# Optimization experiments

Measured on AMD Instinct MI355X. Metric: run time of the kernel, lower is better.

## Reference

```python
import jax, jax.numpy as jnp
import numpy as np

BITS = 12
MB = BITS - 1                      # mantissa bits
MAX_VAL = 1.0 - 2.0 ** (-MB)       # superfloat max representable magnitude
DENOM = float(2 ** MB - 1)


def sf_decode(enc):
    # enc: int32. NOTE: faithful to source, including its sign convention
    # decoded * (2*sign - 1) where sign=1 for negative inputs (flips sign).
    mantissa = enc & ((1 << MB) - 1)
    sign = (enc >> MB) & 1
    mag = mantissa.astype(jnp.float32) / DENOM * MAX_VAL
    return mag * (2 * sign - 1).astype(jnp.float32)


def sf_encode(x):
    c = jnp.clip(x, -MAX_VAL, MAX_VAL)
    oor = jnp.abs(x) > MAX_VAL
    mantissa = jnp.floor(jnp.abs(c) * DENOM / MAX_VAL).astype(jnp.int32)
    sign = (c < 0).astype(jnp.int32)
    return (mantissa | (sign << MB)), oor


def setup_inputs() -> dict:
    key = jax.random.key(0)
    k1, k2, k3, k4, k5 = jax.random.split(key, 5)
    T, IN, OUT = 512, 4096, 11008
    x = jax.random.normal(k1, (T, IN), dtype=jnp.float32)
    weight_full = jax.random.normal(k2, (OUT, IN), dtype=jnp.float32) * 0.02
    scale = jnp.ones((OUT,), dtype=jnp.float32)
    bias = jax.random.normal(k3, (OUT,), dtype=jnp.float32) * 0.01
    encoded_weight = jax.random.randint(k4, (OUT, IN), 0, 2 ** BITS, dtype=jnp.int32)
    outlier_mask = jax.random.uniform(k5, (OUT, IN)) < 0.005
    return {"x": x, "weight_full": weight_full, "scale": scale, "bias": bias,
            "encoded_weight": encoded_weight, "outlier_mask": outlier_mask}


def reference(x, weight_full, scale, bias, encoded_weight, outlier_mask):
    # decode packed superfloat weight, scatter outliers, rescale per-row
    w = sf_decode(encoded_weight)                       # [OUT, IN]
    w = jnp.where(outlier_mask, weight_full, w)         # == w[mask] = weight[mask]
    w = w * scale[:, None]
    # quantize activations (encode then decode)
    enc_x, _ = sf_encode(x)
    xq = sf_decode(enc_x)                               # [T, IN]
    return xq @ w.T + bias                              # [T, OUT]
```

## Files before the change

### kernel.cpp

```cpp
#include <hip/hip_runtime.h>
#include <hip/hip_bf16.h>
#include <stdint.h>

#define T_DIM 512
#define IN_DIM 4096
#define OUT_DIM 11008

typedef __attribute__((ext_vector_type(8))) __bf16 bf16x8;
typedef __attribute__((ext_vector_type(8))) short shortx8;
typedef __attribute__((ext_vector_type(4))) float f32x4;

__device__ __forceinline__ short f32_to_bf16_bits(float f) {
    uint32_t x = __builtin_bit_cast(uint32_t, f);
    x += 0x7FFFu + ((x >> 16) & 1u);
    return (short)(x >> 16);
}

__global__ __launch_bounds__(256) void encode_x_kernel(const float* __restrict__ x,
                                                       short* __restrict__ xq) {
    const float MAXV = 2047.0f / 2048.0f;
    int i = (blockIdx.x * 256 + threadIdx.x) * 8;
    float4 a = *(const float4*)(x + i);
    float4 b = *(const float4*)(x + i + 4);
    float v[8] = {a.x, a.y, a.z, a.w, b.x, b.y, b.z, b.w};
    union { short s[8]; int4 v4; } u;
#pragma unroll
    for (int j = 0; j < 8; ++j) {
        float xv = v[j];
        float ax = fminf(fabsf(xv), MAXV);
        float m = floorf(ax * 2047.0f / MAXV);
        float q = m * (1.0f / 2048.0f) * (xv < 0.0f ? 1.0f : -1.0f);
        u.s[j] = f32_to_bf16_bits(q);
    }
    *(int4*)(xq + i) = u.v4;
}

__global__ __launch_bounds__(256) void decode_w_kernel(const int* __restrict__ enc,
                                                       const int* __restrict__ mask,
                                                       const float* __restrict__ wf,
                                                       const float* __restrict__ scale,
                                                       short* __restrict__ wq) {
    int i = (blockIdx.x * 256 + threadIdx.x) * 8;
    int row = i >> 12;
    float s = scale[row];
    int4 e0 = *(const int4*)(enc + i);
    int4 e1 = *(const int4*)(enc + i + 4);
    int4 m0 = *(const int4*)(mask + i);
    int4 m1 = *(const int4*)(mask + i + 4);
    int e[8]  = {e0.x, e0.y, e0.z, e0.w, e1.x, e1.y, e1.z, e1.w};
    int mk[8] = {m0.x, m0.y, m0.z, m0.w, m1.x, m1.y, m1.z, m1.w};
    union { short s[8]; int4 v4; } u;
#pragma unroll
    for (int j = 0; j < 8; ++j) {
        int ev = e[j];
        float v = (float)(ev & 2047) * (1.0f / 2048.0f) * (((ev >> 11) & 1) ? 1.0f : -1.0f);
        if (mk[j]) v = wf[i + j];
        u.s[j] = f32_to_bf16_bits(v * s);
    }
    *(int4*)(wq + i) = u.v4;
}

#define BM 128
#define BN 128
#define BK 32
#define KITERS (IN_DIM / BK)

__global__ __launch_bounds__(256) void gemm_bt_kernel(const short* __restrict__ A,
                                                      const short* __restrict__ B,
                                                      const float* __restrict__ bias,
                                                      float* __restrict__ C) {
    __shared__ short As[BM * BK];
    __shared__ short Bs[BN * BK];
    const int tid  = threadIdx.x;
    const int wave = tid >> 6;
    const int lane = tid & 63;
    const int bn = blockIdx.x, bm = blockIdx.y;

    const int f0 = tid * 8;
    const int r0 = f0 >> 5, c0 = f0 & 31;
    const int f1 = (256 + tid) * 8;
    const int r1 = f1 >> 5, c1 = f1 & 31;
    const short* gA0 = A + (size_t)(bm * BM + r0) * IN_DIM + c0;
    const short* gA1 = A + (size_t)(bm * BM + r1) * IN_DIM + c1;
    const short* gB0 = B + (size_t)(bn * BN + r0) * IN_DIM + c0;
    const short* gB1 = B + (size_t)(bn * BN + r1) * IN_DIM + c1;
    short* lA0 = As + (wave * 64) * 8;
    short* lA1 = As + (256 + wave * 64) * 8;
    short* lB0 = Bs + (wave * 64) * 8;
    short* lB1 = Bs + (256 + wave * 64) * 8;

    const int wm = (wave >> 1) * 64;
    const int wn = (wave & 1) * 64;
    const int quad = lane >> 4;
    const int lr   = lane & 15;

    f32x4 acc[4][4] = {};

    for (int kt = 0; kt < KITERS; ++kt) {
        const int ko = kt * BK;
        __builtin_amdgcn_global_load_lds((__attribute__((address_space(1))) void*)(gA0 + ko),
                                         (__attribute__((address_space(3))) void*)lA0, 16, 0, 0);
        __builtin_amdgcn_global_load_lds((__attribute__((address_space(1))) void*)(gA1 + ko),
                                         (__attribute__((address_space(3))) void*)lA1, 16, 0, 0);
        __builtin_amdgcn_global_load_lds((__attribute__((address_space(1))) void*)(gB0 + ko),
                                         (__attribute__((address_space(3))) void*)lB0, 16, 0, 0);
        __builtin_amdgcn_global_load_lds((__attribute__((address_space(1))) void*)(gB1 + ko),
                                         (__attribute__((address_space(3))) void*)lB1, 16, 0, 0);
        __syncthreads();

        bf16x8 af[4], bfr[4];
#pragma unroll
        for (int mi = 0; mi < 4; ++mi)
            af[mi] = __builtin_bit_cast(bf16x8,
                *(const shortx8*)(As + (wm + mi * 16 + lr) * BK + quad * 8));
#pragma unroll
        for (int ni = 0; ni < 4; ++ni)
            bfr[ni] = __builtin_bit_cast(bf16x8,
                *(const shortx8*)(Bs + (wn + ni * 16 + lr) * BK + quad * 8));
#pragma unroll
        for (int mi = 0; mi < 4; ++mi)
#pragma unroll
            for (int ni = 0; ni < 4; ++ni)
                acc[mi][ni] = __builtin_amdgcn_mfma_f32_16x16x32_bf16(
                    af[mi], bfr[ni], acc[mi][ni], 0, 0, 0);
        __syncthreads();
    }

    const int rowb = bm * BM + wm + quad * 4;
    const int colb = bn * BN + wn + lr;
#pragma unroll
    for (int ni = 0; ni < 4; ++ni) {
        const int col = colb + ni * 16;
        const float bv = bias[col];
#pragma unroll
        for (int mi = 0; mi < 4; ++mi) {
#pragma unroll
            for (int r = 0; r < 4; ++r) {
                const int row = rowb + mi * 16 + r;
                C[(size_t)row * OUT_DIM + col] = acc[mi][ni][r] + bv;
            }
        }
    }
}

extern "C" void kernel_launch(void* const* d_in, const int* in_sizes, int n_in,
                              void* d_out, int out_size, void* d_ws, size_t ws_size,
                              hipStream_t stream) {
    const float* x     = (const float*)d_in[0];
    const float* wf    = (const float*)d_in[1];
    const float* scale = (const float*)d_in[2];
    const float* bias  = (const float*)d_in[3];
    const int*   enc   = (const int*)d_in[4];
    const int*   mask  = (const int*)d_in[5];
    float* out = (float*)d_out;

    short* xq = (short*)d_ws;
    short* wq = (short*)d_ws + (size_t)T_DIM * IN_DIM;

    encode_x_kernel<<<(T_DIM * IN_DIM) / (256 * 8), 256, 0, stream>>>(x, xq);
    decode_w_kernel<<<((size_t)OUT_DIM * IN_DIM) / (256 * 8), 256, 0, stream>>>(
        enc, mask, wf, scale, wq);
    dim3 grid(OUT_DIM / BN, T_DIM / BM);
    gemm_bt_kernel<<<grid, 256, 0, stream>>>(xq, wq, bias, out);
}
```

Measured before the change: 555.0 us.

## Fuse weight dequantization into GEMM with full-T column blocks

The separate weight-decode kernel and its bf16 workspace round trip are removed. Each block now owns 32 output columns across all 512 tokens: it dequantizes enc/mask/outlier weights into a double-buffered, XOR-swizzled LDS tile while MFMAs consume the previous tile, and it reads activation fragments straight from global memory. The intent is to stream the large int32 weight and mask arrays exactly once, with non-temporal loads, and to overlap that streaming with compute. The cost is that activations are re-read from global/L2 by every one of the 344 blocks, and there are few blocks with high register pressure.

Result: slower. 667.6 us (+20.3%).

```diff
diff --git a/kernel.cpp b/kernel.cpp
--- a/kernel.cpp
+++ b/kernel.cpp
@@ -6,9 +6,15 @@
 #define IN_DIM 4096
 #define OUT_DIM 11008
 
+#define BN 32
+#define BK 64
+#define KSTEPS (IN_DIM / BK)
+#define NBLK (OUT_DIM / BN)
+
 typedef __attribute__((ext_vector_type(8))) __bf16 bf16x8;
 typedef __attribute__((ext_vector_type(8))) short shortx8;
 typedef __attribute__((ext_vector_type(4))) float f32x4;
+typedef __attribute__((ext_vector_type(4))) int   intx4;
 
 __device__ __forceinline__ short f32_to_bf16_bits(float f) {
     uint32_t x = __builtin_bit_cast(uint32_t, f);
@@ -35,105 +41,135 @@
     *(int4*)(xq + i) = u.v4;
 }
 
-__global__ __launch_bounds__(256) void decode_w_kernel(const int* __restrict__ enc,
-                                                       const int* __restrict__ mask,
-                                                       const float* __restrict__ wf,
-                                                       const float* __restrict__ scale,
-                                                       short* __restrict__ wq) {
-    int i = (blockIdx.x * 256 + threadIdx.x) * 8;
-    int row = i >> 12;
-    float s = scale[row];
-    int4 e0 = *(const int4*)(enc + i);
-    int4 e1 = *(const int4*)(enc + i + 4);
-    int4 m0 = *(const int4*)(mask + i);
-    int4 m1 = *(const int4*)(mask + i + 4);
-    int e[8]  = {e0.x, e0.y, e0.z, e0.w, e1.x, e1.y, e1.z, e1.w};
-    int mk[8] = {m0.x, m0.y, m0.z, m0.w, m1.x, m1.y, m1.z, m1.w};
-    union { short s[8]; int4 v4; } u;
-#pragma unroll
-    for (int j = 0; j < 8; ++j) {
-        int ev = e[j];
-        float v = (float)(ev & 2047) * (1.0f / 2048.0f) * (((ev >> 11) & 1) ? 1.0f : -1.0f);
-        if (mk[j]) v = wf[i + j];
-        u.s[j] = f32_to_bf16_bits(v * s);
-    }
-    *(int4*)(wq + i) = u.v4;
-}
+__global__ __launch_bounds__(256, 2) void fused_dq_gemm_kernel(
+    const short* __restrict__ A,
+    const int*   __restrict__ enc,
+    const int*   __restrict__ mask,
+    const float* __restrict__ wf,
+    const float* __restrict__ scale,
+    const float* __restrict__ bias,
+    float*       __restrict__ C)
+{
+    __shared__ short Ws[2][BN * BK];
 
-#define BM 128
-#define BN 128
-#define BK 32
-#define KITERS (IN_DIM / BK)
-
-__global__ __launch_bounds__(256) void gemm_bt_kernel(const short* __restrict__ A,
-                                                      const short* __restrict__ B,
-                                                      const float* __restrict__ bias,
-                                                      float* __restrict__ C) {
-    __shared__ short As[BM * BK];
-    __shared__ short Bs[BN * BK];
     const int tid  = threadIdx.x;
     const int wave = tid >> 6;
     const int lane = tid & 63;
-    const int bn = blockIdx.x, bm = blockIdx.y;
-
-    const int f0 = tid * 8;
-    const int r0 = f0 >> 5, c0 = f0 & 31;
-    const int f1 = (256 + tid) * 8;
-    const int r1 = f1 >> 5, c1 = f1 & 31;
-    const short* gA0 = A + (size_t)(bm * BM + r0) * IN_DIM + c0;
-    const short* gA1 = A + (size_t)(bm * BM + r1) * IN_DIM + c1;
-    const short* gB0 = B + (size_t)(bn * BN + r0) * IN_DIM + c0;
-    const short* gB1 = B + (size_t)(bn * BN + r1) * IN_DIM + c1;
-    short* lA0 = As + (wave * 64) * 8;
-    short* lA1 = As + (256 + wave * 64) * 8;
-    short* lB0 = Bs + (wave * 64) * 8;
-    short* lB1 = Bs + (256 + wave * 64) * 8;
-
-    const int wm = (wave >> 1) * 64;
-    const int wn = (wave & 1) * 64;
     const int quad = lane >> 4;
     const int lr   = lane & 15;
+    const int wm   = wave * 128;
+    const int bn   = blockIdx.x;
 
-    f32x4 acc[4][4] = {};
+    const int wrow = tid >> 3;
+    const int q8   = tid & 7;
+    const int grow = bn * BN + wrow;
+    const float s     = scale[grow];
+    const float s2048 = s * (1.0f / 2048.0f);
+    const int*   ep = enc  + (size_t)grow * IN_DIM + q8 * 8;
+    const int*   mp = mask + (size_t)grow * IN_DIM + q8 * 8;
+    const float* wp = wf   + (size_t)grow * IN_DIM + q8 * 8;
+    char* wsw_base = (char*)&Ws[0][0] +
+        (((wrow * (BK * 2) + q8 * 16) ^ ((wrow & 7) << 4)));
 
-    for (int kt = 0; kt < KITERS; ++kt) {
-        const int ko = kt * BK;
-        __builtin_amdgcn_global_load_lds((__attribute__((address_space(1))) void*)(gA0 + ko),
-                                         (__attribute__((address_space(3))) void*)lA0, 16, 0, 0);
-        __builtin_amdgcn_global_load_lds((__attribute__((address_space(1))) void*)(gA1 + ko),
-                                         (__attribute__((address_space(3))) void*)lA1, 16, 0, 0);
-        __builtin_amdgcn_global_load_lds((__attribute__((address_space(1))) void*)(gB0 + ko),
-                                         (__attribute__((address_space(3))) void*)lB0, 16, 0, 0);
-        __builtin_amdgcn_global_load_lds((__attribute__((address_space(1))) void*)(gB1 + ko),
-                                         (__attribute__((address_space(3))) void*)lB1, 16, 0, 0);
-        __syncthreads();
+    const short* pa = A + (size_t)(wm + lr) * IN_DIM + quad * 8;
 
-        bf16x8 af[4], bfr[4];
+    f32x4 acc[8][2] = {};
+
+    auto WS_FRAG = [&](int rb, int ni, int kf) -> bf16x8 {
+        const int row  = ni * 16 + lr;
+        const int byte = ((row * (BK * 2) + quad * 16 + kf * 64) ^ ((row & 7) << 4))
+                         + rb * (BN * BK * 2);
+        return __builtin_bit_cast(bf16x8, *(const shortx8*)((const char*)&Ws[0][0] + byte));
+    };
+
+    auto DQW = [&](const intx4 E0, const intx4 E1, const int* mv, const float* wv, int wb) {
+        int ev[8] = {E0[0], E0[1], E0[2], E0[3], E1[0], E1[1], E1[2], E1[3]};
+        union { short h[8]; int4 q4; } u;
 #pragma unroll
-        for (int mi = 0; mi < 4; ++mi)
-            af[mi] = __builtin_bit_cast(bf16x8,
-                *(const shortx8*)(As + (wm + mi * 16 + lr) * BK + quad * 8));
+        for (int j = 0; j < 8; ++j) {
+            float d = (float)(ev[j] & 2047);
+            if (!(ev[j] & 2048)) d = -d;
+            float v = d * s2048;
+            if (mv[j]) v = wv[j] * s;
+            u.h[j] = f32_to_bf16_bits(v);
+        }
+        *(int4*)(wsw_base + wb * (BN * BK * 2)) = u.q4;
+    };
+
+    intx4 eA0, eA1, mA0, mA1, eB0, eB1, mB0, mB1;
+    eA0 = __builtin_nontemporal_load((const intx4*)(ep));
+    eA1 = __builtin_nontemporal_load((const intx4*)(ep + 4));
+    mA0 = __builtin_nontemporal_load((const intx4*)(mp));
+    mA1 = __builtin_nontemporal_load((const intx4*)(mp + 4));
+    eB0 = __builtin_nontemporal_load((const intx4*)(ep + BK));
+    eB1 = __builtin_nontemporal_load((const intx4*)(ep + BK + 4));
+    mB0 = __builtin_nontemporal_load((const intx4*)(mp + BK));
+    mB1 = __builtin_nontemporal_load((const intx4*)(mp + BK + 4));
+
+    {
+        int   mv0[8] = {mA0[0], mA0[1], mA0[2], mA0[3], mA1[0], mA1[1], mA1[2], mA1[3]};
+        float wv0[8];
 #pragma unroll
-        for (int ni = 0; ni < 4; ++ni)
-            bfr[ni] = __builtin_bit_cast(bf16x8,
-                *(const shortx8*)(Bs + (wn + ni * 16 + lr) * BK + quad * 8));
-#pragma unroll
-        for (int mi = 0; mi < 4; ++mi)
-#pragma unroll
-            for (int ni = 0; ni < 4; ++ni)
-                acc[mi][ni] = __builtin_amdgcn_mfma_f32_16x16x32_bf16(
-                    af[mi], bfr[ni], acc[mi][ni], 0, 0, 0);
-        __syncthreads();
+        for (int j = 0; j < 8; ++j)
+            if (mv0[j]) wv0[j] = wp[j];
+        DQW(eA0, eA1, mv0, wv0, 0);
+    }
+    __syncthreads();
+
+#define STEP(KT, Ei0, Ei1, Mi0, Mi1, Ed0, Ed1, Md0, Md1, RB, WB)                      \
+    {                                                                                  \
+        const int ko = (KT) * BK;                                                      \
+        bf16x8 af[8][2];                                                               \
+        _Pragma("unroll")                                                              \
+        for (int mi = 0; mi < 8; ++mi) {                                               \
+            const short* p = pa + (size_t)mi * (16 * IN_DIM) + ko;                     \
+            af[mi][0] = __builtin_bit_cast(bf16x8, *(const shortx8*)(p));              \
+            af[mi][1] = __builtin_bit_cast(bf16x8, *(const shortx8*)(p + 32));         \
+        }                                                                              \
+        if ((KT) + 2 < KSTEPS) {                                                       \
+            Ei0 = __builtin_nontemporal_load((const intx4*)(ep + ko + 2 * BK));        \
+            Ei1 = __builtin_nontemporal_load((const intx4*)(ep + ko + 2 * BK + 4));    \
+            Mi0 = __builtin_nontemporal_load((const intx4*)(mp + ko + 2 * BK));        \
+            Mi1 = __builtin_nontemporal_load((const intx4*)(mp + ko + 2 * BK + 4));    \
+        }                                                                              \
+        int mdv[8]; float wv[8];                                                       \
+        if ((KT) + 1 < KSTEPS) {                                                       \
+            mdv[0] = Md0[0]; mdv[1] = Md0[1]; mdv[2] = Md0[2]; mdv[3] = Md0[3];        \
+            mdv[4] = Md1[0]; mdv[5] = Md1[1]; mdv[6] = Md1[2]; mdv[7] = Md1[3];        \
+            _Pragma("unroll")                                                          \
+            for (int j = 0; j < 8; ++j)                                                \
+                if (mdv[j]) wv[j] = wp[ko + BK + j];                                   \
+        }                                                                              \
+        _Pragma("unroll")                                                              \
+        for (int kf = 0; kf < 2; ++kf) {                                               \
+            bf16x8 b0 = WS_FRAG(RB, 0, kf);                                            \
+            bf16x8 b1 = WS_FRAG(RB, 1, kf);                                            \
+            _Pragma("unroll")                                                          \
+            for (int mi = 0; mi < 8; ++mi) {                                           \
+                acc[mi][0] = __builtin_amdgcn_mfma_f32_16x16x32_bf16(af[mi][kf], b0,   \
+                                                                     acc[mi][0], 0, 0, 0); \
+                acc[mi][1] = __builtin_amdgcn_mfma_f32_16x16x32_bf16(af[mi][kf], b1,   \
+                                                                     acc[mi][1], 0, 0, 0); \
+            }                                                                          \
+        }                                                                              \
+        if ((KT) + 1 < KSTEPS) DQW(Ed0, Ed1, mdv, wv, WB);                             \
+        __syncthreads();                                                               \
     }
 
-    const int rowb = bm * BM + wm + quad * 4;
-    const int colb = bn * BN + wn + lr;
+    for (int kt = 0; kt < KSTEPS; kt += 2) {
+        STEP(kt,     eA0, eA1, mA0, mA1, eB0, eB1, mB0, mB1, 0, 1)
+        STEP(kt + 1, eB0, eB1, mB0, mB1, eA0, eA1, mA0, mA1, 1, 0)
+    }
+#undef STEP
+
+    const int rowb = wm + quad * 4;
+    const int colb = bn * BN + lr;
 #pragma unroll
-    for (int ni = 0; ni < 4; ++ni) {
+    for (int ni = 0; ni < 2; ++ni) {
         const int col = colb + ni * 16;
         const float bv = bias[col];
 #pragma unroll
-        for (int mi = 0; mi < 4; ++mi) {
+        for (int mi = 0; mi < 8; ++mi) {
 #pragma unroll
             for (int r = 0; r < 4; ++r) {
                 const int row = rowb + mi * 16 + r;
@@ -147,19 +183,15 @@
                               void* d_out, int out_size, void* d_ws, size_t ws_size,
                               hipStream_t stream) {
     const float* x     = (const float*)d_in[0];
-    const float* wf    = (const float*)d_in[1];
+    const float* wfull = (const float*)d_in[1];
     const float* scale = (const float*)d_in[2];
     const float* bias  = (const float*)d_in[3];
     const int*   enc   = (const int*)d_in[4];
     const int*   mask  = (const int*)d_in[5];
+
     float* out = (float*)d_out;
-
-    short* xq = (short*)d_ws;
-    short* wq = (short*)d_ws + (size_t)T_DIM * IN_DIM;
+    short* xq  = (short*)d_ws;
 
     encode_x_kernel<<<(T_DIM * IN_DIM) / (256 * 8), 256, 0, stream>>>(x, xq);
-    decode_w_kernel<<<((size_t)OUT_DIM * IN_DIM) / (256 * 8), 256, 0, stream>>>(
-        enc, mask, wf, scale, wq);
-    dim3 grid(OUT_DIM / BN, T_DIM / BM);
-    gemm_bt_kernel<<<grid, 256, 0, stream>>>(xq, wq, bias, out);
+    fused_dq_gemm_kernel<<<NBLK, 256, 0, stream>>>(xq, enc, mask, wfull, scale, bias, out);
 }
```
